# Kernel optimization log

Measured on AMD Instinct MI355X. Metric: run time of the kernel, lower is better.

## Reference

```python
import jax, jax.numpy as jnp
import numpy as np

KE_KCAL = 332.0636  # Coulomb constant, kcal/mol * Angstrom / e^2
R_CUT = 5.0
R_ON = R_CUT / 4.0
R_OFF = 3.0 * R_CUT / 4.0
B, A, F = 32, 1024, 128  # molecules, atoms per molecule, feature dim
MAX_Z = 86


def silu(x):
    return x * jax.nn.sigmoid(x)


def res_mlp(x, W1, W2, Wout):
    # Residual (two pre-activation linears) -> activation -> Linear, no biases
    h = silu(x) @ W1
    h = silu(h) @ W2
    return silu(x + h) @ Wout


def f_switch(r):
    # smooth switching function built from sigma(x)=exp(-1/x) for x>0 else 0
    arg = (r - R_ON) / (R_OFF - R_ON)
    def sigma(x):
        xs = jnp.where(x > 0, x, 1.0)
        return jnp.where(x > 0, jnp.exp(-1.0 / xs), 0.0)
    num = sigma(1.0 - arg)
    return num / (num + sigma(arg))


def setup_inputs() -> dict:
    key = jax.random.key(0)
    ks = jax.random.split(key, 16)
    box = 22.0  # ~liquid density box for 1024 atoms (Angstrom)
    s = 1.0 / np.sqrt(F)
    return {
        'e_z': jax.random.normal(ks[0], (B * A, F), jnp.float32) * 0.1,
        'charge': jax.random.normal(ks[1], (B,), jnp.float32),
        'xyz': jax.random.uniform(ks[2], (B, A, 3), jnp.float32) * box,
        'W_lin': jax.random.normal(ks[3], (F, F), jnp.float32) * s,
        'b_lin': jnp.zeros((F,), jnp.float32),
        'k_plus': jax.random.normal(ks[4], (F,), jnp.float32) * s,
        'k_minus': jax.random.normal(ks[5], (F,), jnp.float32) * s,
        'v_plus': jax.random.normal(ks[6], (F,), jnp.float32) * s,
        'v_minus': jax.random.normal(ks[7], (F,), jnp.float32) * s,
        'Wr1': jax.random.normal(ks[8], (F, F), jnp.float32) * s,
        'Wr2': jax.random.normal(ks[9], (F, F), jnp.float32) * s,
        'Wout': jax.random.normal(ks[10], (F, F), jnp.float32) * s,
        'w_e': jax.random.normal(ks[11], (F,), jnp.float32) * s,
        'q_z_table': jax.random.normal(ks[12], (MAX_Z,), jnp.float32) * 0.01,
        'z': jax.random.randint(ks[13], (B * A,), 1, MAX_Z, jnp.int32),
    }


def reference(e_z, charge, xyz, W_lin, b_lin, k_plus, k_minus, v_plus, v_minus,
              Wr1, Wr2, Wout, w_e, q_z_table, z):
    # ---- ElectronicEmbedding (per-molecule loop vectorized over B) ----
    q = (e_z @ W_lin + b_lin).reshape(B, A, F)
    pos = (charge >= 0)[:, None]                       # [B,1]
    k = jnp.where(pos, k_plus[None, :], k_minus[None, :])   # [B,F]
    v = jnp.where(pos, v_plus[None, :], v_minus[None, :])   # [B,F]
    arg = jnp.einsum('baf,bf->ba', q, k) / np.sqrt(F)
    num = jax.nn.softplus(arg)                         # log(1+exp)
    a = charge[:, None] * num / num.sum(axis=1, keepdims=True)  # [B,A]
    av = a[:, :, None] * v[:, None, :]                 # [B,A,F]
    e_psi = res_mlp(av.reshape(B * A, F), Wr1, Wr2, Wout)
    f = e_z + e_psi                                    # atom features [N,F]

    # ---- Electrostatics.get_charge (charge-conserving correction) ----
    pred_q = (f @ w_e + q_z_table[z]).reshape(B, A)
    corr = (charge - pred_q.sum(axis=1)) / A
    q_atom = pred_q + corr[:, None]                    # [B,A]

    # ---- Electrostatics.get_en: O(A^2) pairwise switched Coulomb ----
    diff = xyz[:, :, None, :] - xyz[:, None, :, :]     # [B,A,A,3]
    r2 = jnp.sum(diff * diff, axis=-1)                 # [B,A,A]
    mask = jnp.triu(jnp.ones((A, A), bool), k=1)       # pairs j > i (r>0)
    r = jnp.sqrt(jnp.where(mask, r2, 1.0))
    fs = f_switch(r)
    coul = fs / jnp.sqrt(r * r + 1.0) + (1.0 - fs) / r
    pair_e = q_atom[:, :, None] * q_atom[:, None, :] * coul
    energy = KE_KCAL * jnp.sum(jnp.where(mask, pair_e, 0.0), axis=(1, 2))  # [B]
    return energy
```

## Files before the change

kernel.cpp:

```cpp
#include <hip/hip_runtime.h>
#include <math.h>

#define B_MOL 32
#define A_AT  1024
#define NF    128
#define N_AT  (B_MOL * A_AT)

#define WS_K2P     0
#define WS_K2M     128
#define WS_WOUT    256
#define WS_C       384
#define WS_NUMSUM  512
#define WS_PREDSUM 544
#define WS_NUM     1024
#define WS_EZWE    (WS_NUM + N_AT)
#define WS_PRED    (WS_EZWE + N_AT)
#define WS_SIDX    (WS_PRED + N_AT)
#define WS_SPOS    (WS_SIDX + N_AT)

__device__ __forceinline__ float fast_rcp(float x) { return __builtin_amdgcn_rcpf(x); }
__device__ __forceinline__ float fast_rsq(float x) { return __builtin_amdgcn_rsqf(x); }
__device__ __forceinline__ float silu_f(float x) { return x * fast_rcp(1.f + __expf(-x)); }

__device__ __forceinline__ float wave_sum(float v) {
#pragma unroll
  for (int o = 32; o > 0; o >>= 1) v += __shfl_xor(v, o, 64);
  return v;
}

__global__ void pre_kernel(const float* __restrict__ W_lin, const float* __restrict__ b_lin,
                           const float* __restrict__ k_plus, const float* __restrict__ k_minus,
                           const float* __restrict__ Wout, const float* __restrict__ w_e,
                           float* __restrict__ ws, float* __restrict__ out) {
  int g = threadIdx.x;
  if (blockIdx.x == 0) {
    float sp = 0.f, sm = 0.f;
    for (int f = 0; f < NF; f++) {
      float wl = W_lin[g * NF + f];
      sp = fmaf(wl, k_plus[f], sp);
      sm = fmaf(wl, k_minus[f], sm);
    }
    ws[WS_K2P + g] = sp;
    ws[WS_K2M + g] = sm;
  } else {
    float sw = 0.f;
    for (int f = 0; f < NF; f++) sw = fmaf(Wout[g * NF + f], w_e[f], sw);
    ws[WS_WOUT + g] = sw;
    if (g < 2) {
      const float* kk = (g == 0) ? k_plus : k_minus;
      float c = 0.f;
      for (int f = 0; f < NF; f++) c = fmaf(b_lin[f], kk[f], c);
      ws[WS_C + g] = c;
    }
    if (g < 64) ws[WS_NUMSUM + g] = 0.f;
    if (g < 32) out[g] = 0.f;
  }
}

__global__ __launch_bounds__(256) void sort_kernel(const float* __restrict__ xyz,
                                                   float* __restrict__ ws) {
  int mol = blockIdx.x, tid = threadIdx.x;
  __shared__ int hist[64], start[64];
  if (tid < 64) hist[tid] = 0;
  __syncthreads();
  float px[4], py[4], pz[4];
  int cell[4];
#pragma unroll
  for (int r = 0; r < 4; r++) {
    int j = tid + r * 256;
    const float* p = xyz + (size_t)(mol * A_AT + j) * 3;
    px[r] = p[0]; py[r] = p[1]; pz[r] = p[2];
    int cx = min(3, max(0, (int)(px[r] * (4.f / 22.f))));
    int cy = min(3, max(0, (int)(py[r] * (4.f / 22.f))));
    int cz = min(3, max(0, (int)(pz[r] * (4.f / 22.f))));
    cell[r] = cx * 16 + cy * 4 + cz;
    atomicAdd(&hist[cell[r]], 1);
  }
  __syncthreads();
  if (tid == 0) {
    int s = 0;
    for (int c = 0; c < 64; c++) { start[c] = s; s += hist[c]; }
  }
  __syncthreads();
  float4* spos = (float4*)(ws + WS_SPOS);
  int* sidx = (int*)ws + WS_SIDX;
#pragma unroll
  for (int r = 0; r < 4; r++) {
    int j = tid + r * 256;
    int off = atomicAdd(&start[cell[r]], 1);
    int g = mol * A_AT + off;
    spos[g] = make_float4(px[r], py[r], pz[r], 0.f);
    sidx[g] = j;
  }
}

__global__ __launch_bounds__(128) void attn_kernel(const float* __restrict__ e_z,
                                                   const float* __restrict__ charge,
                                                   const float* __restrict__ w_e,
                                                   float* __restrict__ ws) {
  int bx = blockIdx.x;
  int mol = bx >> 3;
  int n = mol * A_AT + (bx & 7) * 128 + threadIdx.x;
  __shared__ float k2[NF], wesh[NF];
  float ch = charge[mol];
  const float* k2src = ws + (ch >= 0.f ? WS_K2P : WS_K2M);
  k2[threadIdx.x] = k2src[threadIdx.x];
  wesh[threadIdx.x] = w_e[threadIdx.x];
  float cc = ws[WS_C + (ch >= 0.f ? 0 : 1)];
  __syncthreads();
  const float4* row = (const float4*)(e_z + (size_t)n * NF);
  float dk = 0.f, dw = 0.f;
#pragma unroll 8
  for (int i = 0; i < NF / 4; i++) {
    float4 v = row[i];
    dk = fmaf(v.x, k2[4*i+0], dk); dk = fmaf(v.y, k2[4*i+1], dk);
    dk = fmaf(v.z, k2[4*i+2], dk); dk = fmaf(v.w, k2[4*i+3], dk);
    dw = fmaf(v.x, wesh[4*i+0], dw); dw = fmaf(v.y, wesh[4*i+1], dw);
    dw = fmaf(v.z, wesh[4*i+2], dw); dw = fmaf(v.w, wesh[4*i+3], dw);
  }
  float arg = (dk + cc) * 0.08838834764831845f;
  float num = fmaxf(arg, 0.f) + log1pf(__expf(-fabsf(arg)));
  ws[WS_NUM + n] = num;
  ws[WS_EZWE + n] = dw;
  float s = wave_sum(num);
  if ((threadIdx.x & 63) == 0) atomicAdd(&ws[WS_NUMSUM + mol], s);
}

__global__ __launch_bounds__(256, 4) void mlp_kernel(const float* __restrict__ charge,
                                                     const float* __restrict__ v_plus,
                                                     const float* __restrict__ v_minus,
                                                     const float* __restrict__ Wr1,
                                                     const float* __restrict__ Wr2,
                                                     const int* __restrict__ z,
                                                     const float* __restrict__ qz_table,
                                                     float* __restrict__ ws) {
  int base = blockIdx.x * 32;
  int mol = base >> 10;
  int tid = threadIdx.x;
  int tx = tid & 15, ty = tid >> 4;

  __shared__ float Wch[32 * 128];
  __shared__ float sxch[32 * 34];
  __shared__ float vsh[128], wout_sh[128], awsh[32], pred_sh[32];

  float ch = charge[mol];
  if (tid < 128) {
    vsh[tid] = (ch >= 0.f) ? v_plus[tid] : v_minus[tid];
    wout_sh[tid] = ws[WS_WOUT + tid];
  }
  if (tid < 32) awsh[tid] = ch * ws[WS_NUM + base + tid] / ws[WS_NUMSUM + mol];

  float acc[2][8], acc2[2][8];
#pragma unroll
  for (int i = 0; i < 2; i++)
#pragma unroll
    for (int j = 0; j < 8; j++) { acc[i][j] = 0.f; acc2[i][j] = 0.f; }

  for (int c = 0; c < 4; c++) {
    __syncthreads();
    const float4* wsrc = (const float4*)(Wr1 + c * 32 * NF);
    float4* wdst = (float4*)Wch;
#pragma unroll
    for (int r = 0; r < 4; r++) wdst[tid + r * 256] = wsrc[tid + r * 256];
#pragma unroll
    for (int r = 0; r < 4; r++) {
      int idx = tid + r * 256;
      int kk = idx >> 5, m = idx & 31;
      sxch[kk * 34 + m] = silu_f(awsh[m] * vsh[c * 32 + kk]);
    }
    __syncthreads();
#pragma unroll 8
    for (int kk = 0; kk < 32; kk++) {
      float2 a = *(const float2*)&sxch[kk * 34 + ty * 2];
      float4 b0 = *(const float4*)&Wch[kk * 128 + tx * 4];
      float4 b1 = *(const float4*)&Wch[kk * 128 + 64 + tx * 4];
      float am[2] = {a.x, a.y};
      float bm[8] = {b0.x, b0.y, b0.z, b0.w, b1.x, b1.y, b1.z, b1.w};
#pragma unroll
      for (int mi = 0; mi < 2; mi++)
#pragma unroll
        for (int fj = 0; fj < 8; fj++)
          acc[mi][fj] = fmaf(am[mi], bm[fj], acc[mi][fj]);
    }
  }

  for (int c = 0; c < 4; c++) {
    __syncthreads();
    const float4* wsrc = (const float4*)(Wr2 + c * 32 * NF);
    float4* wdst = (float4*)Wch;
#pragma unroll
    for (int r = 0; r < 4; r++) wdst[tid + r * 256] = wsrc[tid + r * 256];
    if ((tx >> 3) == (c & 1)) {
      int fb = (c < 2) ? 0 : 4;
#pragma unroll
      for (int f2 = 0; f2 < 4; f2++) {
        int k = (tx & 7) * 4 + f2;
        sxch[k * 34 + ty * 2 + 0] = silu_f(acc[0][fb + f2]);
        sxch[k * 34 + ty * 2 + 1] = silu_f(acc[1][fb + f2]);
      }
    }
    __syncthreads();
#pragma unroll 8
    for (int kk = 0; kk < 32; kk++) {
      float2 a = *(const float2*)&sxch[kk * 34 + ty * 2];
      float4 b0 = *(const float4*)&Wch[kk * 128 + tx * 4];
      float4 b1 = *(const float4*)&Wch[kk * 128 + 64 + tx * 4];
      float am[2] = {a.x, a.y};
      float bm[8] = {b0.x, b0.y, b0.z, b0.w, b1.x, b1.y, b1.z, b1.w};
#pragma unroll
      for (int mi = 0; mi < 2; mi++)
#pragma unroll
        for (int fj = 0; fj < 8; fj++)
          acc2[mi][fj] = fmaf(am[mi], bm[fj], acc2[mi][fj]);
    }
  }

  float partial[2] = {0.f, 0.f};
#pragma unroll
  for (int mi = 0; mi < 2; mi++) {
    float aw = awsh[ty * 2 + mi];
#pragma unroll
    for (int fj = 0; fj < 8; fj++) {
      int f = (fj < 4) ? (tx * 4 + fj) : (64 + tx * 4 + fj - 4);
      float s = silu_f(fmaf(aw, vsh[f], acc2[mi][fj]));
      partial[mi] = fmaf(s, wout_sh[f], partial[mi]);
    }
  }
#pragma unroll
  for (int o = 8; o > 0; o >>= 1) {
    partial[0] += __shfl_xor(partial[0], o, 64);
    partial[1] += __shfl_xor(partial[1], o, 64);
  }
  if (tx == 0) {
#pragma unroll
    for (int mi = 0; mi < 2; mi++) {
      int m = ty * 2 + mi;
      int n = base + m;
      float pred = partial[mi] + ws[WS_EZWE + n] + qz_table[z[n]];
      ws[WS_PRED + n] = pred;
      pred_sh[m] = pred;
    }
  }
  __syncthreads();
  if (tid < 64) {
    float v = (tid < 32) ? pred_sh[tid] : 0.f;
    float s = wave_sum(v);
    if (tid == 0) atomicAdd(&ws[WS_PREDSUM + mol], s);
  }
}

__global__ __launch_bounds__(512) void pair_kernel(const float* __restrict__ xyz,
                                                   const float* __restrict__ charge,
                                                   float* __restrict__ ws,
                                                   float* __restrict__ out) {
  int bx = blockIdx.x;
  int mol = bx >> 4;
  int sub = bx & 15;
  int tid = threadIdx.x;
  __shared__ float4 posq[1024];
  __shared__ float wred[8];
  const float4* spos = (const float4*)(ws + WS_SPOS);
  const int* sidx = (const int*)ws + WS_SIDX;
  float corr = (charge[mol] - ws[WS_PREDSUM + mol]) * (1.f / 1024.f);
  for (int j = tid; j < 1024; j += 512) {
    float4 p = spos[mol * 1024 + j];
    p.w = ws[WS_PRED + mol * 1024 + sidx[mol * 1024 + j]] + corr;
    posq[j] = p;
  }
  __syncthreads();
  int i = sub * 64 + (tid & 63);
  int jq = tid >> 6;
  float4 me = posq[i];
  float e = 0.f;
  int j0 = jq * 128;
#pragma unroll 2
  for (int j = j0; j < j0 + 128; j++) {
    float4 p = posq[j];
    float dx = me.x - p.x, dy = me.y - p.y, dz = me.z - p.z;
    float r2 = fmaf(dx, dx, fmaf(dy, dy, dz * dz));
    bool self = (j == i);
    if (self) r2 = 1.0e8f;
    float qj = self ? 0.f : p.w;
    float inv_r = fast_rsq(r2);
    e = fmaf(qj, inv_r, e);
    if (__any(r2 < 14.0625f)) {
      float r = r2 * inv_r;
      float arg = (r - 1.25f) * 0.4f;
      float argc = fminf(fmaxf(arg, 1e-6f), 1.f - 1e-6f);
      float t = fast_rcp(argc) - fast_rcp(1.f - argc);
      float fs = fast_rcp(1.f + __expf(-t));
      float delta = fs * (fast_rsq(r2 + 1.f) - inv_r);
      e = fmaf(qj, delta, e);
    }
  }
  e *= me.w;
  float s = wave_sum(e);
  if ((tid & 63) == 0) wred[tid >> 6] = s;
  __syncthreads();
  if (tid == 0) {
    float tot = 0.f;
#pragma unroll
    for (int k = 0; k < 8; k++) tot += wred[k];
    atomicAdd(&out[mol], 166.0318f * tot);
  }
}

extern "C" void kernel_launch(void* const* d_in, const int* in_sizes, int n_in,
                              void* d_out, int out_size, void* d_ws, size_t ws_size,
                              hipStream_t stream) {
  const float* e_z     = (const float*)d_in[0];
  const float* charge  = (const float*)d_in[1];
  const float* xyz     = (const float*)d_in[2];
  const float* W_lin   = (const float*)d_in[3];
  const float* b_lin   = (const float*)d_in[4];
  const float* k_plus  = (const float*)d_in[5];
  const float* k_minus = (const float*)d_in[6];
  const float* v_plus  = (const float*)d_in[7];
  const float* v_minus = (const float*)d_in[8];
  const float* Wr1     = (const float*)d_in[9];
  const float* Wr2     = (const float*)d_in[10];
  const float* Wout    = (const float*)d_in[11];
  const float* w_e     = (const float*)d_in[12];
  const float* qz      = (const float*)d_in[13];
  const int*   z       = (const int*)d_in[14];
  float* out = (float*)d_out;
  float* ws  = (float*)d_ws;

  pre_kernel<<<2, 128, 0, stream>>>(W_lin, b_lin, k_plus, k_minus, Wout, w_e, ws, out);
  sort_kernel<<<32, 256, 0, stream>>>(xyz, ws);
  attn_kernel<<<256, 128, 0, stream>>>(e_z, charge, w_e, ws);
  mlp_kernel<<<1024, 256, 0, stream>>>(charge, v_plus, v_minus, Wr1, Wr2, z, qz, ws);
  pair_kernel<<<512, 512, 0, stream>>>(xyz, charge, ws, out);
}
```

Before: 170.4 us.

## Use bf16 MFMA for residual MLP with prepacked weight fragments

The two 128x128 residual MLP matmuls move from FP32 FMA loops to bf16 MFMA 16x16x32 instructions. Wr1 and Wr2 are converted to bf16 and laid out in fragment order once, in pre_kernel. The MLP block now handles 64 atoms per block with one wave per 16 rows. The attention projection also splits each row across four lanes to give more parallelism. This cuts the FP32 ALU cost of the MLP but adds bf16 rounding error to the predicted charges and the energy.

```diff
diff --git a/kernel.cpp b/kernel.cpp
--- a/kernel.cpp
+++ b/kernel.cpp
@@ -17,43 +17,78 @@
 #define WS_PRED    (WS_EZWE + N_AT)
 #define WS_SIDX    (WS_PRED + N_AT)
 #define WS_SPOS    (WS_SIDX + N_AT)
+#define WS_W1F     (WS_SPOS + 4 * N_AT)
+#define WS_W2F     (WS_W1F + 8192)
+
+typedef short short8 __attribute__((ext_vector_type(8)));
+typedef float floatx4 __attribute__((ext_vector_type(4)));
 
 __device__ __forceinline__ float fast_rcp(float x) { return __builtin_amdgcn_rcpf(x); }
 __device__ __forceinline__ float fast_rsq(float x) { return __builtin_amdgcn_rsqf(x); }
 __device__ __forceinline__ float silu_f(float x) { return x * fast_rcp(1.f + __expf(-x)); }
 
+__device__ __forceinline__ short f2bf(float x) {
+  unsigned u = __float_as_uint(x);
+  u += 0x7fffu + ((u >> 16) & 1u);
+  return (short)(u >> 16);
+}
+
 __device__ __forceinline__ float wave_sum(float v) {
 #pragma unroll
   for (int o = 32; o > 0; o >>= 1) v += __shfl_xor(v, o, 64);
   return v;
 }
 
-__global__ void pre_kernel(const float* __restrict__ W_lin, const float* __restrict__ b_lin,
-                           const float* __restrict__ k_plus, const float* __restrict__ k_minus,
-                           const float* __restrict__ Wout, const float* __restrict__ w_e,
-                           float* __restrict__ ws, float* __restrict__ out) {
-  int g = threadIdx.x;
-  if (blockIdx.x == 0) {
-    float sp = 0.f, sm = 0.f;
-    for (int f = 0; f < NF; f++) {
-      float wl = W_lin[g * NF + f];
-      sp = fmaf(wl, k_plus[f], sp);
-      sm = fmaf(wl, k_minus[f], sm);
-    }
-    ws[WS_K2P + g] = sp;
-    ws[WS_K2M + g] = sm;
+__global__ __launch_bounds__(256) void pre_kernel(const float* __restrict__ W_lin,
+                                                  const float* __restrict__ b_lin,
+                                                  const float* __restrict__ k_plus,
+                                                  const float* __restrict__ k_minus,
+                                                  const float* __restrict__ Wout,
+                                                  const float* __restrict__ w_e,
+                                                  const float* __restrict__ Wr1,
+                                                  const float* __restrict__ Wr2,
+                                                  float* __restrict__ ws,
+                                                  float* __restrict__ out) {
+  int tid = threadIdx.x;
+  if (blockIdx.x < 2) {
+    const float* W = (blockIdx.x == 0) ? Wr1 : Wr2;
+    short* dst = (short*)(ws + ((blockIdx.x == 0) ? WS_W1F : WS_W2F));
+#pragma unroll
+    for (int it = 0; it < 8; it++) {
+      int idx = it * 256 + tid;
+      int fi = idx >> 6, lane = idx & 63;
+      int nt = fi >> 2, ks = fi & 3;
+      int q = lane >> 4, n15 = lane & 15;
+      int k0 = ks * 32 + q * 8;
+      int col = nt * 16 + n15;
+#pragma unroll
+      for (int j = 0; j < 8; j++)
+        dst[fi * 512 + lane * 8 + j] = f2bf(W[(k0 + j) * NF + col]);
+    }
   } else {
-    float sw = 0.f;
-    for (int f = 0; f < NF; f++) sw = fmaf(Wout[g * NF + f], w_e[f], sw);
-    ws[WS_WOUT + g] = sw;
-    if (g < 2) {
-      const float* kk = (g == 0) ? k_plus : k_minus;
-      float c = 0.f;
-      for (int f = 0; f < NF; f++) c = fmaf(b_lin[f], kk[f], c);
-      ws[WS_C + g] = c;
-    }
-    if (g < 64) ws[WS_NUMSUM + g] = 0.f;
-    if (g < 32) out[g] = 0.f;
+    if (tid < 128) {
+      float sp = 0.f, sm = 0.f;
+      for (int f = 0; f < NF; f++) {
+        float wl = W_lin[tid * NF + f];
+        sp = fmaf(wl, k_plus[f], sp);
+        sm = fmaf(wl, k_minus[f], sm);
+      }
+      ws[WS_K2P + tid] = sp;
+      ws[WS_K2M + tid] = sm;
+      if (tid < 2) {
+        const float* kk = (tid == 0) ? k_plus : k_minus;
+        float c = 0.f;
+        for (int f = 0; f < NF; f++) c = fmaf(b_lin[f], kk[f], c);
+        ws[WS_C + tid] = c;
+      }
+    } else {
+      int g = tid - 128;
+      float sw = 0.f;
+      for (int f = 0; f < NF; f++) sw = fmaf(Wout[g * NF + f], w_e[f], sw);
+      ws[WS_WOUT + g] = sw;
+      if (g < 64) ws[WS_NUMSUM + g] = 0.f;
+      if (g < 32) out[g] = 0.f;
+    }
   }
 }
 
@@ -94,157 +129,165 @@
   }
 }
 
-__global__ __launch_bounds__(128) void attn_kernel(const float* __restrict__ e_z,
+__global__ __launch_bounds__(256) void attn_kernel(const float* __restrict__ e_z,
                                                    const float* __restrict__ charge,
                                                    const float* __restrict__ w_e,
                                                    float* __restrict__ ws) {
-  int bx = blockIdx.x;
-  int mol = bx >> 3;
-  int n = mol * A_AT + (bx & 7) * 128 + threadIdx.x;
+  int tid = threadIdx.x;
+  int t = blockIdx.x * 256 + tid;
+  int n = t >> 2;
+  int part = t & 3;
+  int mol = blockIdx.x >> 4;
   __shared__ float k2[NF], wesh[NF];
   float ch = charge[mol];
-  const float* k2src = ws + (ch >= 0.f ? WS_K2P : WS_K2M);
-  k2[threadIdx.x] = k2src[threadIdx.x];
-  wesh[threadIdx.x] = w_e[threadIdx.x];
+  if (tid < 128) {
+    const float* k2src = ws + (ch >= 0.f ? WS_K2P : WS_K2M);
+    k2[tid] = k2src[tid];
+    wesh[tid] = w_e[tid];
+  }
   float cc = ws[WS_C + (ch >= 0.f ? 0 : 1)];
   __syncthreads();
-  const float4* row = (const float4*)(e_z + (size_t)n * NF);
+  const float4* row = (const float4*)(e_z + (size_t)n * NF + part * 32);
   float dk = 0.f, dw = 0.f;
 #pragma unroll 8
-  for (int i = 0; i < NF / 4; i++) {
+  for (int i = 0; i < 8; i++) {
     float4 v = row[i];
-    dk = fmaf(v.x, k2[4*i+0], dk); dk = fmaf(v.y, k2[4*i+1], dk);
-    dk = fmaf(v.z, k2[4*i+2], dk); dk = fmaf(v.w, k2[4*i+3], dk);
-    dw = fmaf(v.x, wesh[4*i+0], dw); dw = fmaf(v.y, wesh[4*i+1], dw);
-    dw = fmaf(v.z, wesh[4*i+2], dw); dw = fmaf(v.w, wesh[4*i+3], dw);
-  }
-  float arg = (dk + cc) * 0.08838834764831845f;
-  float num = fmaxf(arg, 0.f) + log1pf(__expf(-fabsf(arg)));
-  ws[WS_NUM + n] = num;
-  ws[WS_EZWE + n] = dw;
+    int b = part * 32 + i * 4;
+    dk = fmaf(v.x, k2[b+0], dk); dk = fmaf(v.y, k2[b+1], dk);
+    dk = fmaf(v.z, k2[b+2], dk); dk = fmaf(v.w, k2[b+3], dk);
+    dw = fmaf(v.x, wesh[b+0], dw); dw = fmaf(v.y, wesh[b+1], dw);
+    dw = fmaf(v.z, wesh[b+2], dw); dw = fmaf(v.w, wesh[b+3], dw);
+  }
+  dk += __shfl_xor(dk, 1, 64); dk += __shfl_xor(dk, 2, 64);
+  dw += __shfl_xor(dw, 1, 64); dw += __shfl_xor(dw, 2, 64);
+  float num = 0.f;
+  if (part == 0) {
+    float arg = (dk + cc) * 0.08838834764831845f;
+    num = fmaxf(arg, 0.f) + log1pf(__expf(-fabsf(arg)));
+    ws[WS_NUM + n] = num;
+    ws[WS_EZWE + n] = dw;
+  }
   float s = wave_sum(num);
-  if ((threadIdx.x & 63) == 0) atomicAdd(&ws[WS_NUMSUM + mol], s);
-}
-
-__global__ __launch_bounds__(256, 4) void mlp_kernel(const float* __restrict__ charge,
-                                                     const float* __restrict__ v_plus,
-                                                     const float* __restrict__ v_minus,
-                                                     const float* __restrict__ Wr1,
-                                                     const float* __restrict__ Wr2,
-                                                     const int* __restrict__ z,
-                                                     const float* __restrict__ qz_table,
-                                                     float* __restrict__ ws) {
-  int base = blockIdx.x * 32;
+  if ((tid & 63) == 0) atomicAdd(&ws[WS_NUMSUM + mol], s);
+}
+
+__global__ __launch_bounds__(256) void mlp_kernel(const float* __restrict__ charge,
+                                                  const float* __restrict__ v_plus,
+                                                  const float* __restrict__ v_minus,
+                                                  const int* __restrict__ z,
+                                                  const float* __restrict__ qz_table,
+                                                  float* __restrict__ ws) {
+  int base = blockIdx.x * 64;
   int mol = base >> 10;
   int tid = threadIdx.x;
-  int tx = tid & 15, ty = tid >> 4;
-
-  __shared__ float Wch[32 * 128];
-  __shared__ float sxch[32 * 34];
-  __shared__ float vsh[128], wout_sh[128], awsh[32], pred_sh[32];
+  int w = tid >> 6;
+  int lane = tid & 63;
+  int q = lane >> 4, l15 = lane & 15;
+
+  __shared__ short wf[16384];
+  __shared__ short a2s[4 * 16 * 136];
+  __shared__ float vsh[NF], wout_sh[NF], awsh[64], pred_sh[64];
 
   float ch = charge[mol];
   if (tid < 128) {
     vsh[tid] = (ch >= 0.f) ? v_plus[tid] : v_minus[tid];
     wout_sh[tid] = ws[WS_WOUT + tid];
   }
-  if (tid < 32) awsh[tid] = ch * ws[WS_NUM + base + tid] / ws[WS_NUMSUM + mol];
-
-  float acc[2][8], acc2[2][8];
-#pragma unroll
-  for (int i = 0; i < 2; i++)
-#pragma unroll
-    for (int j = 0; j < 8; j++) { acc[i][j] = 0.f; acc2[i][j] = 0.f; }
-
-  for (int c = 0; c < 4; c++) {
-    __syncthreads();
-    const float4* wsrc = (const float4*)(Wr1 + c * 32 * NF);
-    float4* wdst = (float4*)Wch;
-#pragma unroll
-    for (int r = 0; r < 4; r++) wdst[tid + r * 256] = wsrc[tid + r * 256];
+  if (tid < 64) awsh[tid] = ch * ws[WS_NUM + base + tid] / ws[WS_NUMSUM + mol];
+
+  {
+    const float4* src = (const float4*)(ws + WS_W1F);
+    float4* dst = (float4*)wf;
+#pragma unroll
+    for (int r = 0; r < 8; r++) dst[tid + r * 256] = src[tid + r * 256];
+  }
+  __syncthreads();
+
+  float aw_m = awsh[w * 16 + l15];
+  floatx4 acc1[8];
+#pragma unroll
+  for (int nt = 0; nt < 8; nt++) acc1[nt] = (floatx4)(0.f);
+
+#pragma unroll
+  for (int ks = 0; ks < 4; ks++) {
+    float4 va = *(const float4*)&vsh[ks * 32 + q * 8];
+    float4 vb = *(const float4*)&vsh[ks * 32 + q * 8 + 4];
+    short8 af;
+    af[0] = f2bf(silu_f(aw_m * va.x)); af[1] = f2bf(silu_f(aw_m * va.y));
+    af[2] = f2bf(silu_f(aw_m * va.z)); af[3] = f2bf(silu_f(aw_m * va.w));
+    af[4] = f2bf(silu_f(aw_m * vb.x)); af[5] = f2bf(silu_f(aw_m * vb.y));
+    af[6] = f2bf(silu_f(aw_m * vb.z)); af[7] = f2bf(silu_f(aw_m * vb.w));
+#pragma unroll
+    for (int nt = 0; nt < 8; nt++) {
+      short8 bf = *(const short8*)&wf[(nt * 4 + ks) * 512 + lane * 8];
+      acc1[nt] = __builtin_amdgcn_mfma_f32_16x16x32_bf16(af, bf, acc1[nt], 0, 0, 0);
+    }
+  }
+
+#pragma unroll
+  for (int nt = 0; nt < 8; nt++) {
+    int f = nt * 16 + l15;
+#pragma unroll
+    for (int r = 0; r < 4; r++)
+      a2s[w * 2176 + (q * 4 + r) * 136 + f] = f2bf(silu_f(acc1[nt][r]));
+  }
+  __syncthreads();
+  {
+    const float4* src = (const float4*)(ws + WS_W2F);
+    float4* dst = (float4*)wf;
+#pragma unroll
+    for (int r = 0; r < 8; r++) dst[tid + r * 256] = src[tid + r * 256];
+  }
+  __syncthreads();
+
+  floatx4 acc2[8];
+#pragma unroll
+  for (int nt = 0; nt < 8; nt++) acc2[nt] = (floatx4)(0.f);
+
+#pragma unroll
+  for (int ks = 0; ks < 4; ks++) {
+    short8 af = *(const short8*)&a2s[w * 2176 + l15 * 136 + ks * 32 + q * 8];
+#pragma unroll
+    for (int nt = 0; nt < 8; nt++) {
+      short8 bf = *(const short8*)&wf[(nt * 4 + ks) * 512 + lane * 8];
+      acc2[nt] = __builtin_amdgcn_mfma_f32_16x16x32_bf16(af, bf, acc2[nt], 0, 0, 0);
+    }
+  }
+
+  float awq[4], part[4];
+#pragma unroll
+  for (int r = 0; r < 4; r++) {
+    awq[r] = awsh[w * 16 + q * 4 + r];
+    part[r] = 0.f;
+  }
+#pragma unroll
+  for (int nt = 0; nt < 8; nt++) {
+    int f = nt * 16 + l15;
+    float vv = vsh[f], ww = wout_sh[f];
 #pragma unroll
     for (int r = 0; r < 4; r++) {
-      int idx = tid + r * 256;
-      int kk = idx >> 5, m = idx & 31;
-      sxch[kk * 34 + m] = silu_f(awsh[m] * vsh[c * 32 + kk]);
-    }
-    __syncthreads();
-#pragma unroll 8
-    for (int kk = 0; kk < 32; kk++) {
-      float2 a = *(const float2*)&sxch[kk * 34 + ty * 2];
-      float4 b0 = *(const float4*)&Wch[kk * 128 + tx * 4];
-      float4 b1 = *(const float4*)&Wch[kk * 128 + 64 + tx * 4];
-      float am[2] = {a.x, a.y};
-      float bm[8] = {b0.x, b0.y, b0.z, b0.w, b1.x, b1.y, b1.z, b1.w};
-#pragma unroll
-      for (int mi = 0; mi < 2; mi++)
-#pragma unroll
-        for (int fj = 0; fj < 8; fj++)
-          acc[mi][fj] = fmaf(am[mi], bm[fj], acc[mi][fj]);
-    }
-  }
-
-  for (int c = 0; c < 4; c++) {
-    __syncthreads();
-    const float4* wsrc = (const float4*)(Wr2 + c * 32 * NF);
-    float4* wdst = (float4*)Wch;
-#pragma unroll
-    for (int r = 0; r < 4; r++) wdst[tid + r * 256] = wsrc[tid + r * 256];
-    if ((tx >> 3) == (c & 1)) {
-      int fb = (c < 2) ? 0 : 4;
-#pragma unroll
-      for (int f2 = 0; f2 < 4; f2++) {
-        int k = (tx & 7) * 4 + f2;
-        sxch[k * 34 + ty * 2 + 0] = silu_f(acc[0][fb + f2]);
-        sxch[k * 34 + ty * 2 + 1] = silu_f(acc[1][fb + f2]);
-      }
-    }
-    __syncthreads();
-#pragma unroll 8
-    for (int kk = 0; kk < 32; kk++) {
-      float2 a = *(const float2*)&sxch[kk * 34 + ty * 2];
-      float4 b0 = *(const float4*)&Wch[kk * 128 + tx * 4];
-      float4 b1 = *(const float4*)&Wch[kk * 128 + 64 + tx * 4];
-      float am[2] = {a.x, a.y};
-      float bm[8] = {b0.x, b0.y, b0.z, b0.w, b1.x, b1.y, b1.z, b1.w};
-#pragma unroll
-      for (int mi = 0; mi < 2; mi++)
-#pragma unroll
-        for (int fj = 0; fj < 8; fj++)
-          acc2[mi][fj] = fmaf(am[mi], bm[fj], acc2[mi][fj]);
-    }
-  }
-
-  float partial[2] = {0.f, 0.f};
-#pragma unroll
-  for (int mi = 0; mi < 2; mi++) {
-    float aw = awsh[ty * 2 + mi];
-#pragma unroll
-    for (int fj = 0; fj < 8; fj++) {
-      int f = (fj < 4) ? (tx * 4 + fj) : (64 + tx * 4 + fj - 4);
-      float s = silu_f(fmaf(aw, vsh[f], acc2[mi][fj]));
-      partial[mi] = fmaf(s, wout_sh[f], partial[mi]);
-    }
-  }
-#pragma unroll
-  for (int o = 8; o > 0; o >>= 1) {
-    partial[0] += __shfl_xor(partial[0], o, 64);
-    partial[1] += __shfl_xor(partial[1], o, 64);
-  }
-  if (tx == 0) {
-#pragma unroll
-    for (int mi = 0; mi < 2; mi++) {
-      int m = ty * 2 + mi;
+      float s = silu_f(fmaf(awq[r], vv, acc2[nt][r]));
+      part[r] = fmaf(s, ww, part[r]);
+    }
+  }
+#pragma unroll
+  for (int r = 0; r < 4; r++) {
+#pragma unroll
+    for (int o = 1; o < 16; o <<= 1) part[r] += __shfl_xor(part[r], o, 64);
+  }
+  if (l15 == 0) {
+#pragma unroll
+    for (int r = 0; r < 4; r++) {
+      int m = w * 16 + q * 4 + r;
       int n = base + m;
-      float pred = partial[mi] + ws[WS_EZWE + n] + qz_table[z[n]];
+      float pred = part[r] + ws[WS_EZWE + n] + qz_table[z[n]];
       ws[WS_PRED + n] = pred;
       pred_sh[m] = pred;
     }
   }
   __syncthreads();
   if (tid < 64) {
-    float v = (tid < 32) ? pred_sh[tid] : 0.f;
-    float s = wave_sum(v);
+    float s = wave_sum(pred_sh[tid]);
     if (tid == 0) atomicAdd(&ws[WS_PREDSUM + mol], s);
   }
 }
@@ -326,9 +369,10 @@
   float* out = (float*)d_out;
   float* ws  = (float*)d_ws;
 
-  pre_kernel<<<2, 128, 0, stream>>>(W_lin, b_lin, k_plus, k_minus, Wout, w_e, ws, out);
+  pre_kernel<<<3, 256, 0, stream>>>(W_lin, b_lin, k_plus, k_minus, Wout, w_e,
+                                    Wr1, Wr2, ws, out);
   sort_kernel<<<32, 256, 0, stream>>>(xyz, ws);
-  attn_kernel<<<256, 128, 0, stream>>>(e_z, charge, w_e, ws);
-  mlp_kernel<<<1024, 256, 0, stream>>>(charge, v_plus, v_minus, Wr1, Wr2, z, qz, ws);
+  attn_kernel<<<512, 256, 0, stream>>>(e_z, charge, w_e, ws);
+  mlp_kernel<<<512, 256, 0, stream>>>(charge, v_plus, v_minus, z, qz, ws);
   pair_kernel<<<512, 512, 0, stream>>>(xyz, charge, ws, out);
 }
```

After: 159.0 us. 1.07x faster.
